# Kernel tuning notes

Measured on AMD Instinct MI355X. Metric: run time of the kernel, lower is better.

## Reference

```python
import jax, jax.numpy as jnp
import numpy as np

HEADS = 16

def _layernorm_LC(x, eps=1e-05):
    # Normalizes jointly over the last TWO dims (L, C), matching the custom LayerNorm.
    mean = jnp.mean(x, axis=(-2, -1), keepdims=True)
    var = jnp.mean((x - mean) ** 2, axis=(-2, -1), keepdims=True) + eps
    return (x - mean) / jnp.sqrt(var)  # affine is identity (ones/zeros)


def setup_inputs() -> dict:
    key = jax.random.key(0)
    ks = jax.random.split(key, 11)
    B, L, D = 2, 2048, 1024
    H = 4 * D
    s = 0.02
    return {
        'x': jax.random.normal(ks[0], (B, L, D), jnp.float32),
        'wq': jax.random.normal(ks[1], (D, D), jnp.float32) * s,
        'bq': jax.random.normal(ks[2], (D,), jnp.float32) * s,
        'wk': jax.random.normal(ks[3], (D, D), jnp.float32) * s,
        'bk': jax.random.normal(ks[4], (D,), jnp.float32) * s,
        'wv': jax.random.normal(ks[5], (D, D), jnp.float32) * s,
        'bv': jax.random.normal(ks[6], (D,), jnp.float32) * s,
        'w1': jax.random.normal(ks[7], (D, H), jnp.float32) * s,
        'b1': jax.random.normal(ks[8], (H,), jnp.float32) * s,
        'w2': jax.random.normal(ks[9], (H, D), jnp.float32) * s,
        'b2': jax.random.normal(ks[10], (D,), jnp.float32) * s,
    }


def reference(x, wq, bq, wk, bk, wv, bv, w1, b1, w2, b2):
    B, L, D = x.shape
    dh = D // HEADS
    # QKV projections
    q = (x @ wq + bq).reshape(B, L, HEADS, dh)
    k = (x @ wk + bk).reshape(B, L, HEADS, dh)
    v = (x @ wv + bv).reshape(B, L, HEADS, dh)
    # batched multi-head attention (equivalent to the per-head Python loop)
    scale = 1.0 / jnp.sqrt(jnp.float32(dh))
    scores = jnp.einsum('blhd,bmhd->bhlm', q, k) * scale
    attn = jax.nn.softmax(scores, axis=-1)
    out = jnp.einsum('bhlm,bmhd->blhd', attn, v).reshape(B, L, D)
    # residual + (L,C) layernorm
    h = _layernorm_LC(x + out)
    # feedforward (dropout is identity in eval)
    ff = jax.nn.relu(h @ w1 + b1) @ w2 + b2
    return _layernorm_LC(h + ff)
```

## Files before the change

kernel.cpp:

```cpp
#include <hip/hip_runtime.h>
#include <hip/hip_bf16.h>

typedef __hip_bfloat16 bf16;
typedef __attribute__((ext_vector_type(8))) short short8;
typedef __attribute__((ext_vector_type(4))) short short4v;
typedef __attribute__((ext_vector_type(4))) float f32x4;

#define CB 2
#define CL 2048
#define CD 1024
#define CH 4096
#define NHEADS 16
#define DH 64

__device__ __forceinline__ short f2bs(float f) {
    __hip_bfloat16 h = __float2bfloat16(f);
    return *reinterpret_cast<short*>(&h);
}
__device__ __forceinline__ float bs2f(short s) {
    __hip_bfloat16 h = *reinterpret_cast<__hip_bfloat16*>(&s);
    return __bfloat162float(h);
}

__device__ __forceinline__ void async_copy16(const short* g, short* l) {
    __builtin_amdgcn_global_load_lds((const __attribute__((address_space(1))) unsigned int*)g,
                                     (__attribute__((address_space(3))) unsigned int*)l,
                                     16, 0, 0);
}

__global__ void pack_bias_kernel(const float* __restrict__ bq, const float* __restrict__ bk,
                                 const float* __restrict__ bv, float* __restrict__ o,
                                 float* __restrict__ stats) {
    int i = blockIdx.x * 256 + threadIdx.x;
    if (i < 16) stats[i] = 0.0f;
    if (i < 3072) o[i] = i < 1024 ? bq[i] : (i < 2048 ? bk[i - 1024] : bv[i - 2048]);
}

__global__ void cvt_x_kernel(const float* __restrict__ x, short* __restrict__ o) {
    const int i = (blockIdx.x * 256 + threadIdx.x) * 4;
    const float4 v = *(const float4*)&x[i];
    short4v s; s[0] = f2bs(v.x); s[1] = f2bs(v.y); s[2] = f2bs(v.z); s[3] = f2bs(v.w);
    *(short4v*)&o[i] = s;
}

__global__ void transpose_cvt(const float* __restrict__ in, short* __restrict__ out,
                              int K, int N, int row_off) {
    __shared__ float T[32][33];
    const int tx = threadIdx.x & 31, ty = threadIdx.x >> 5;
    const int k0 = blockIdx.y * 32, n0 = blockIdx.x * 32;
    #pragma unroll
    for (int i = 0; i < 4; ++i)
        T[ty + i * 8][tx] = in[(size_t)(k0 + ty + i * 8) * N + n0 + tx];
    __syncthreads();
    #pragma unroll
    for (int i = 0; i < 4; ++i)
        out[(size_t)(row_off + n0 + ty + i * 8) * K + k0 + tx] = f2bs(T[tx][ty + i * 8]);
}

__global__ void transpose_qkv(const float* __restrict__ wq, const float* __restrict__ wk,
                              const float* __restrict__ wv, short* __restrict__ out) {
    __shared__ float T[32][33];
    const int z = blockIdx.z;
    const float* in = z == 0 ? wq : (z == 1 ? wk : wv);
    const int row_off = z * 1024;
    const int tx = threadIdx.x & 31, ty = threadIdx.x >> 5;
    const int k0 = blockIdx.y * 32, n0 = blockIdx.x * 32;
    #pragma unroll
    for (int i = 0; i < 4; ++i)
        T[ty + i * 8][tx] = in[(size_t)(k0 + ty + i * 8) * CD + n0 + tx];
    __syncthreads();
    #pragma unroll
    for (int i = 0; i < 4; ++i)
        out[(size_t)(row_off + n0 + ty + i * 8) * CD + k0 + tx] = f2bs(T[tx][ty + i * 8]);
}

template <int BN, int BK, int RELU, int EPI>
__launch_bounds__(256)
__global__ void gemm_mfma(const short* __restrict__ A,
                          const short* __restrict__ Bt,
                          const float* __restrict__ bias,
                          short* __restrict__ C,
                          short* __restrict__ C2,
                          int M, int N, int K,
                          float* __restrict__ stats) {
    constexpr int NT = BN / 32;
    constexpr int KH = BK / 32;
    constexpr int ACH = 16 * BK;
    constexpr int BCH = BN * BK / 8;
    __shared__ short As[128 * BK];
    __shared__ short Bs[BN * BK];
    __shared__ float red[8];

    const int tid = threadIdx.x;
    const int wave = tid >> 6, lane = tid & 63, quad = lane >> 4, lm = lane & 15;
    const int wm = (wave & 1) * 64, wn = (wave >> 1) * (NT * 16);

    const int id = blockIdx.y * gridDim.x + blockIdx.x;
    const int xcd = id & 7, within = id >> 3;
    const int by = xcd * 4 + (within & 3);
    const int bx = within >> 2;
    const int row0 = by * 128, col0 = bx * BN;

    f32x4 acc[4][NT];
    #pragma unroll
    for (int i = 0; i < 4; ++i)
        #pragma unroll
        for (int j = 0; j < NT; ++j) { f32x4 z = {0.f, 0.f, 0.f, 0.f}; acc[i][j] = z; }

    for (int k0 = 0; k0 < K; k0 += BK) {
        #pragma unroll
        for (int t = 0; t < ACH / 256; ++t) {
            const int c = t * 256 + tid;
            const int slab = c >> 9, idx = c & 511;
            const int r = idx >> 2, seg = idx & 3;
            async_copy16(A + (size_t)(row0 + r) * K + k0 + slab * 32 + seg * 8, &As[c * 8]);
        }
        #pragma unroll
        for (int t = 0; t < BCH / 256; ++t) {
            const int c = t * 256 + tid;
            const int slab = c / (BN * 4), idx = c % (BN * 4);
            const int r = idx >> 2, seg = idx & 3;
            async_copy16(Bt + (size_t)(col0 + r) * K + k0 + slab * 32 + seg * 8, &Bs[c * 8]);
        }
        __syncthreads();

        #pragma unroll
        for (int kh = 0; kh < KH; ++kh) {
            short8 af[4], bfr[NT];
            #pragma unroll
            for (int mt = 0; mt < 4; ++mt)
                af[mt] = *(const short8*)&As[kh * 4096 + (wm + mt * 16 + lm) * 32 + quad * 8];
            #pragma unroll
            for (int nt = 0; nt < NT; ++nt)
                bfr[nt] = *(const short8*)&Bs[kh * (BN * 32) + (wn + nt * 16 + lm) * 32 + quad * 8];
            #pragma unroll
            for (int mt = 0; mt < 4; ++mt)
                #pragma unroll
                for (int nt = 0; nt < NT; ++nt)
                    acc[mt][nt] = __builtin_amdgcn_mfma_f32_16x16x32_bf16(af[mt], bfr[nt], acc[mt][nt], 0, 0, 0);
        }
        __syncthreads();
    }

    float s1 = 0.f, s2 = 0.f;
    #pragma unroll
    for (int mt = 0; mt < 4; ++mt) {
        #pragma unroll
        for (int nt = 0; nt < NT; ++nt) {
            const int col = col0 + wn + nt * 16 + lm;
            const float bv = bias[col];
            const int rowb = row0 + wm + mt * 16 + quad * 4;
            if (EPI == 1 && col >= 2048) {
                const int b = row0 >> 11;
                const int l0 = rowb & (CL - 1);
                short4v sv;
                #pragma unroll
                for (int r = 0; r < 4; ++r) sv[r] = f2bs(acc[mt][nt][r] + bv);
                *(short4v*)&C2[(size_t)b * CD * CL + (size_t)(col - 2048) * CL + l0] = sv;
            } else {
                #pragma unroll
                for (int r = 0; r < 4; ++r) {
                    float v = acc[mt][nt][r] + bv;
                    if (RELU) v = fmaxf(v, 0.f);
                    const int ld = (EPI == 1) ? 2048 : N;
                    const size_t idx = (size_t)(rowb + r) * ld + col;
                    if (EPI == 2) {
                        v += bs2f(C[idx]);
                        s1 += v; s2 += v * v;
                    }
                    C[idx] = f2bs(v);
                }
            }
        }
    }
    if (EPI == 2) {
        #pragma unroll
        for (int off = 1; off <= 32; off <<= 1) {
            s1 += __shfl_xor(s1, off, 64);
            s2 += __shfl_xor(s2, off, 64);
        }
        if (lane == 0) { red[wave] = s1; red[4 + wave] = s2; }
        __syncthreads();
        if (tid == 0) {
            const int batch = row0 >> 11;
            atomicAdd(&stats[batch * 2 + 0], red[0] + red[1] + red[2] + red[3]);
            atomicAdd(&stats[batch * 2 + 1], red[4] + red[5] + red[6] + red[7]);
        }
    }
}

__launch_bounds__(256)
__global__ void attn_mfma(const short* __restrict__ qk,
                          const short* __restrict__ vT,
                          const float* __restrict__ x,
                          short* __restrict__ sbuf,
                          float* __restrict__ stats) {
    __shared__ short Ks[64 * 64];
    __shared__ short Vt[64 * 66];
    __shared__ float red[8];

    const int tid = threadIdx.x;
    const int wave = tid >> 6, lane = tid & 63, quad = lane >> 4, lm = lane & 15;

    const int id = blockIdx.z * (16 * 16) + blockIdx.y * 16 + blockIdx.x;
    const int xcd = id & 7, rest = id >> 3;
    const int qx = rest & 15, gq = rest >> 4;
    const int g = gq * 8 + xcd;
    const int h = g & 15, b = g >> 4;

    const int hoff = h * DH;
    const size_t rowb = (size_t)b * CL;
    const size_t vbase = (size_t)b * CD * CL + (size_t)hoff * CL;
    const int qbase0 = qx * 128 + wave * 32;

    short8 bq[2][2];
    #pragma unroll
    for (int qt = 0; qt < 2; ++qt)
        #pragma unroll
        for (int kf = 0; kf < 2; ++kf)
            bq[qt][kf] = *(const short8*)(qk + (rowb + qbase0 + qt * 16 + lm) * 2048 + hoff + kf * 32 + quad * 8);

    f32x4 oacc[2][4];
    #pragma unroll
    for (int qt = 0; qt < 2; ++qt)
        #pragma unroll
        for (int mt = 0; mt < 4; ++mt) { f32x4 z = {0.f, 0.f, 0.f, 0.f}; oacc[qt][mt] = z; }
    float lsum[2] = {0.f, 0.f};

    for (int kt = 0; kt < CL / 64; ++kt) {
        #pragma unroll
        for (int t = 0; t < 2; ++t) {
            const int c = tid + t * 256;
            const int key = c >> 3, seg = c & 7;
            async_copy16(qk + (rowb + kt * 64 + key) * 2048 + 1024 + hoff + seg * 8, &Ks[c * 8]);
        }
        #pragma unroll
        for (int t = 0; t < 2; ++t) {
            const int c = tid + t * 256;
            const int row = c >> 3, seg = c & 7;
            const short8 vv = *(const short8*)(vT + vbase + (size_t)row * CL + kt * 64 + seg * 8);
            *(short8*)&Vt[row * 66 + seg * 8] = vv;
        }
        __syncthreads();

        float st[2][4][4];
        #pragma unroll
        for (int ktile = 0; ktile < 4; ++ktile) {
            const short8 a0 = *(const short8*)&Ks[(ktile * 16 + lm) * 64 + quad * 8];
            const short8 a1 = *(const short8*)&Ks[(ktile * 16 + lm) * 64 + 32 + quad * 8];
            #pragma unroll
            for (int qt = 0; qt < 2; ++qt) {
                f32x4 s = {0.f, 0.f, 0.f, 0.f};
                s = __builtin_amdgcn_mfma_f32_16x16x32_bf16(a0, bq[qt][0], s, 0, 0, 0);
                s = __builtin_amdgcn_mfma_f32_16x16x32_bf16(a1, bq[qt][1], s, 0, 0, 0);
                #pragma unroll
                for (int r = 0; r < 4; ++r) {
                    const float p = __expf(s[r] * 0.125f);
                    lsum[qt] += p;
                    st[qt][ktile][r] = p;
                }
            }
        }

        #pragma unroll
        for (int p = 0; p < 2; ++p) {
            short8 pf[2];
            #pragma unroll
            for (int qt = 0; qt < 2; ++qt)
                #pragma unroll
                for (int r = 0; r < 4; ++r) {
                    pf[qt][r]     = f2bs(st[qt][2 * p][r]);
                    pf[qt][4 + r] = f2bs(st[qt][2 * p + 1][r]);
                }
            #pragma unroll
            for (int mt = 0; mt < 4; ++mt) {
                const int vr = (mt * 16 + lm) * 66 + p * 32 + quad * 4;
                const short4v vlo = *(const short4v*)&Vt[vr];
                const short4v vhi = *(const short4v*)&Vt[vr + 16];
                short8 vf;
                vf[0] = vlo[0]; vf[1] = vlo[1]; vf[2] = vlo[2]; vf[3] = vlo[3];
                vf[4] = vhi[0]; vf[5] = vhi[1]; vf[6] = vhi[2]; vf[7] = vhi[3];
                #pragma unroll
                for (int qt = 0; qt < 2; ++qt)
                    oacc[qt][mt] = __builtin_amdgcn_mfma_f32_16x16x32_bf16(vf, pf[qt], oacc[qt][mt], 0, 0, 0);
            }
        }
        __syncthreads();
    }

    #pragma unroll
    for (int qt = 0; qt < 2; ++qt) {
        lsum[qt] += __shfl_xor(lsum[qt], 16, 64);
        lsum[qt] += __shfl_xor(lsum[qt], 32, 64);
    }

    float s1 = 0.f, s2 = 0.f;
    #pragma unroll
    for (int qt = 0; qt < 2; ++qt) {
        const float inv = 1.0f / lsum[qt];
        const size_t grow = rowb + qbase0 + qt * 16 + lm;
        #pragma unroll
        for (int mt = 0; mt < 4; ++mt) {
            const size_t base = grow * CD + hoff + mt * 16 + quad * 4;
            const float4 xv = *(const float4*)&x[base];
            const float xa[4] = {xv.x, xv.y, xv.z, xv.w};
            short4v sv;
            #pragma unroll
            for (int r = 0; r < 4; ++r) {
                const float s = xa[r] + oacc[qt][mt][r] * inv;
                s1 += s; s2 += s * s;
                sv[r] = f2bs(s);
            }
            *(short4v*)&sbuf[base] = sv;
        }
    }
    #pragma unroll
    for (int off = 1; off <= 32; off <<= 1) {
        s1 += __shfl_xor(s1, off, 64);
        s2 += __shfl_xor(s2, off, 64);
    }
    if (lane == 0) { red[wave] = s1; red[4 + wave] = s2; }
    __syncthreads();
    if (tid == 0) {
        atomicAdd(&stats[b * 2 + 0], red[0] + red[1] + red[2] + red[3]);
        atomicAdd(&stats[b * 2 + 1], red[4] + red[5] + red[6] + red[7]);
    }
}

template <typename TO>
__global__ void ln_apply(const short* __restrict__ s, const float* __restrict__ stats,
                         TO* __restrict__ out, int perBatch) {
    const int bId = blockIdx.y;
    const size_t base = (size_t)bId * perBatch;
    const float n = (float)perBatch;
    const float mean = stats[bId * 2 + 0] / n;
    const float var  = stats[bId * 2 + 1] / n - mean * mean + 1e-5f;
    const float inv  = rsqrtf(var);
    const int stride = gridDim.x * 256 * 8;
    for (int i = (blockIdx.x * 256 + threadIdx.x) * 8; i < perBatch; i += stride) {
        const short8 v8 = *(const short8*)&s[base + i];
        float o[8];
        #pragma unroll
        for (int j = 0; j < 8; ++j) o[j] = (bs2f(v8[j]) - mean) * inv;
        if (sizeof(TO) == 4) {
            float4 f0 = {o[0], o[1], o[2], o[3]}, f1 = {o[4], o[5], o[6], o[7]};
            *(float4*)&((float*)out)[base + i] = f0;
            *(float4*)&((float*)out)[base + i + 4] = f1;
        } else {
            short8 r;
            #pragma unroll
            for (int j = 0; j < 8; ++j) r[j] = f2bs(o[j]);
            *(short8*)&((short*)out)[base + i] = r;
        }
    }
}

extern "C" void kernel_launch(void* const* d_in, const int* in_sizes, int n_in,
                              void* d_out, int out_size, void* d_ws, size_t ws_size,
                              hipStream_t stream) {
    const float* x  = (const float*)d_in[0];
    const float* wq = (const float*)d_in[1];
    const float* bq = (const float*)d_in[2];
    const float* wk = (const float*)d_in[3];
    const float* bk = (const float*)d_in[4];
    const float* wv = (const float*)d_in[5];
    const float* bv = (const float*)d_in[6];
    const float* w1 = (const float*)d_in[7];
    const float* b1 = (const float*)d_in[8];
    const float* w2 = (const float*)d_in[9];
    const float* b2 = (const float*)d_in[10];

    const int BL = CB * CL;
    const int perBatch = CL * CD;

    char* ws = (char*)d_ws;
    const size_t MB = 1024 * 1024;
    short* Wqkvt = (short*)(ws);
    float* bqkv  = (float*)(ws + 6 * MB);
    short* w1t   = (short*)(ws);
    short* w2t   = (short*)(ws);
    short* xbf   = (short*)(ws + 8 * MB);
    short* qkb   = (short*)(ws + 16 * MB);
    short* vT    = (short*)(ws + 32 * MB);
    short* ff1   = (short*)(ws + 8 * MB);
    short* hbuf  = (short*)(ws + 40 * MB);
    float* stats = (float*)(ws + 48 * MB);

    dim3 blk(256);

    pack_bias_kernel<<<12, blk, 0, stream>>>(bq, bk, bv, bqkv, stats);
    cvt_x_kernel<<<BL * CD / 1024, blk, 0, stream>>>(x, xbf);
    transpose_qkv<<<dim3(32, 32, 3), blk, 0, stream>>>(wq, wk, wv, Wqkvt);

    gemm_mfma<128, 64, 0, 1><<<dim3(3072 / 128, BL / 128), blk, 0, stream>>>(
        xbf, Wqkvt, bqkv, qkb, vT, BL, 3072, CD, nullptr);

    attn_mfma<<<dim3(CL / 128, NHEADS, CB), blk, 0, stream>>>(qkb, vT, x, hbuf, stats);

    ln_apply<bf16><<<dim3(128, CB), blk, 0, stream>>>(hbuf, stats, (bf16*)hbuf, perBatch);

    transpose_cvt<<<dim3(128, 32), blk, 0, stream>>>(w1, w1t, CD, CH, 0);
    gemm_mfma<128, 64, 1, 0><<<dim3(CH / 128, BL / 128), blk, 0, stream>>>(
        hbuf, w1t, b1, ff1, nullptr, BL, CH, CD, nullptr);

    transpose_cvt<<<dim3(32, 128), blk, 0, stream>>>(w2, w2t, CH, CD, 0);
    gemm_mfma<64, 128, 0, 2><<<dim3(CD / 64, BL / 128), blk, 0, stream>>>(
        ff1, w2t, b2, hbuf, nullptr, BL, CD, CH, stats + 8);

    ln_apply<float><<<dim3(128, CB), blk, 0, stream>>>(hbuf, stats + 8, (float*)d_out, perBatch);
}
```

Baseline: 357.1 us.

## Double-buffer K/V tiles with async copies and XOR-swizzled LDS in attention

The attention kernel now keeps two LDS buffers for K and V and issues asynchronous global-to-LDS copies for the next key tile while the current one is being computed. This is meant to hide load latency and drop one barrier per iteration. V is also loaded with async copies instead of register round-trips, and both tiles use an XOR swizzle in place of padding to avoid LDS bank conflicts. The MFMA sections are wrapped in s_setprio to favour matrix issue. LDS use doubles, and correctness depends on async-copy completion being ordered by the remaining single barrier.

```diff
diff --git a/kernel.cpp b/kernel.cpp
--- a/kernel.cpp
+++ b/kernel.cpp
@@ -195,12 +195,13 @@
                           const float* __restrict__ x,
                           short* __restrict__ sbuf,
                           float* __restrict__ stats) {
-    __shared__ short Ks[64 * 64];
-    __shared__ short Vt[64 * 66];
+    __shared__ short Ks[2][64 * 64];
+    __shared__ short Vs[2][64 * 64];
     __shared__ float red[8];
 
     const int tid = threadIdx.x;
     const int wave = tid >> 6, lane = tid & 63, quad = lane >> 4, lm = lane & 15;
+    const int sx = lm & 7;
 
     const int id = blockIdx.z * (16 * 16) + blockIdx.y * 16 + blockIdx.x;
     const int xcd = id & 7, rest = id >> 3;
@@ -227,39 +228,57 @@
         for (int mt = 0; mt < 4; ++mt) { f32x4 z = {0.f, 0.f, 0.f, 0.f}; oacc[qt][mt] = z; }
     float lsum[2] = {0.f, 0.f};
 
-    for (int kt = 0; kt < CL / 64; ++kt) {
+    auto stage = [&](int buf, int kt) {
         #pragma unroll
         for (int t = 0; t < 2; ++t) {
             const int c = tid + t * 256;
-            const int key = c >> 3, seg = c & 7;
-            async_copy16(qk + (rowb + kt * 64 + key) * 2048 + 1024 + hoff + seg * 8, &Ks[c * 8]);
+            const int key = c >> 3, sp = c & 7;
+            async_copy16(qk + (rowb + kt * 64 + key) * 2048 + 1024 + hoff + ((sp ^ (key & 7)) * 8),
+                         &Ks[buf][c * 8]);
         }
         #pragma unroll
         for (int t = 0; t < 2; ++t) {
             const int c = tid + t * 256;
-            const int row = c >> 3, seg = c & 7;
-            const short8 vv = *(const short8*)(vT + vbase + (size_t)row * CL + kt * 64 + seg * 8);
-            *(short8*)&Vt[row * 66 + seg * 8] = vv;
-        }
-        __syncthreads();
+            const int row = c >> 3, sp = c & 7;
+            async_copy16(vT + vbase + (size_t)row * CL + kt * 64 + ((sp ^ (row & 7)) * 8),
+                         &Vs[buf][c * 8]);
+        }
+    };
+
+    stage(0, 0);
+    __syncthreads();
+    int cur = 0;
+
+    for (int kt = 0; kt < CL / 64; ++kt) {
+        if (kt + 1 < CL / 64) stage(cur ^ 1, kt + 1);
+        const short* K_ = &Ks[cur][0];
+        const short* V_ = &Vs[cur][0];
 
         float st[2][4][4];
         #pragma unroll
         for (int ktile = 0; ktile < 4; ++ktile) {
-            const short8 a0 = *(const short8*)&Ks[(ktile * 16 + lm) * 64 + quad * 8];
-            const short8 a1 = *(const short8*)&Ks[(ktile * 16 + lm) * 64 + 32 + quad * 8];
+            const int krow = ktile * 16 + lm;
+            const int s0 = (quad ^ sx) << 3;
+            const short8 a0 = *(const short8*)&K_[krow * 64 + s0];
+            const short8 a1 = *(const short8*)&K_[krow * 64 + (s0 ^ 32)];
+            f32x4 sv[2];
+            __builtin_amdgcn_s_setprio(1);
             #pragma unroll
             for (int qt = 0; qt < 2; ++qt) {
                 f32x4 s = {0.f, 0.f, 0.f, 0.f};
                 s = __builtin_amdgcn_mfma_f32_16x16x32_bf16(a0, bq[qt][0], s, 0, 0, 0);
                 s = __builtin_amdgcn_mfma_f32_16x16x32_bf16(a1, bq[qt][1], s, 0, 0, 0);
+                sv[qt] = s;
+            }
+            __builtin_amdgcn_s_setprio(0);
+            #pragma unroll
+            for (int qt = 0; qt < 2; ++qt)
                 #pragma unroll
                 for (int r = 0; r < 4; ++r) {
-                    const float p = __expf(s[r] * 0.125f);
+                    const float p = __expf(sv[qt][r] * 0.125f);
                     lsum[qt] += p;
                     st[qt][ktile][r] = p;
                 }
-            }
         }
 
         #pragma unroll
@@ -274,18 +293,23 @@
                 }
             #pragma unroll
             for (int mt = 0; mt < 4; ++mt) {
-                const int vr = (mt * 16 + lm) * 66 + p * 32 + quad * 4;
-                const short4v vlo = *(const short4v*)&Vt[vr];
-                const short4v vhi = *(const short4v*)&Vt[vr + 16];
+                const int vrow = mt * 16 + lm;
+                const int sc = (p * 4 + (quad >> 1)) ^ sx;
+                const int vb = vrow * 64 + (quad & 1) * 4;
+                const short4v vlo = *(const short4v*)&V_[vb + sc * 8];
+                const short4v vhi = *(const short4v*)&V_[vb + (sc ^ 2) * 8];
                 short8 vf;
                 vf[0] = vlo[0]; vf[1] = vlo[1]; vf[2] = vlo[2]; vf[3] = vlo[3];
                 vf[4] = vhi[0]; vf[5] = vhi[1]; vf[6] = vhi[2]; vf[7] = vhi[3];
+                __builtin_amdgcn_s_setprio(1);
                 #pragma unroll
                 for (int qt = 0; qt < 2; ++qt)
                     oacc[qt][mt] = __builtin_amdgcn_mfma_f32_16x16x32_bf16(vf, pf[qt], oacc[qt][mt], 0, 0, 0);
+                __builtin_amdgcn_s_setprio(0);
             }
         }
         __syncthreads();
+        cur ^= 1;
     }
 
     #pragma unroll
```

Result: faster. 349.0 us (-2.3%).
